# Optimization experiments

Measured on AMD Instinct MI355X. Metric: run time of the kernel, lower is better.

## Reference

```python
import jax, jax.numpy as jnp
import numpy as np
from jax import lax

N = 100000      # number of nodes (== ninput)
E = 3200000     # number of edges per adjacency
NHID = 128
EPS = 1e-12     # torch F.normalize eps


def spmm(src, dst, w, x):
    # sparse adj @ x : out[i] = sum_{e: dst[e]==i} w[e] * x[src[e]]
    return jax.ops.segment_sum(w[:, None] * x[src], dst, num_segments=N)


def l2norm(x):
    # F.normalize(x, p=2, dim=1)
    n = jnp.sqrt(jnp.sum(x * x, axis=1, keepdims=True))
    return x / jnp.maximum(n, EPS)


def mlp(x, L1, bl1, L2, bl2, L3, bl3):
    # dropout == 0.0 -> identity; chunking is a memory optimization, same math
    h = jax.nn.relu(x @ L1 + bl1)
    h = jax.nn.relu(h @ L2 + bl2)
    return h @ L3 + bl3  # [N, 1]


def setup_inputs() -> dict:
    key = jax.random.key(0)
    ks = jax.random.split(key, 32)
    d = {}
    d["adj1_src"] = jax.random.randint(ks[0], (E,), 0, N, dtype=jnp.int32)
    d["adj1_dst"] = jax.random.randint(ks[1], (E,), 0, N, dtype=jnp.int32)
    d["adj1_w"] = jax.random.uniform(ks[2], (E,), dtype=jnp.float32)
    d["adj2_src"] = jax.random.randint(ks[3], (E,), 0, N, dtype=jnp.int32)
    d["adj2_dst"] = jax.random.randint(ks[4], (E,), 0, N, dtype=jnp.int32)
    d["adj2_w"] = jax.random.uniform(ks[5], (E,), dtype=jnp.float32)
    d["W1"] = jax.random.normal(ks[6], (N, NHID), dtype=jnp.float32) * 0.05
    d["b1"] = jnp.zeros((NHID,), jnp.float32)
    for i, k in zip(range(2, 7), ks[7:12]):
        d[f"W{i}"] = jax.random.normal(k, (NHID, NHID), dtype=jnp.float32) * (1.0 / np.sqrt(NHID))
        d[f"b{i}"] = jnp.zeros((NHID,), jnp.float32)
    d["L1"] = jax.random.normal(ks[12], (NHID, 2 * NHID), dtype=jnp.float32) * (1.0 / np.sqrt(NHID))
    d["bl1"] = jnp.zeros((2 * NHID,), jnp.float32)
    d["L2"] = jax.random.normal(ks[13], (2 * NHID, 2 * NHID), dtype=jnp.float32) * (1.0 / np.sqrt(2 * NHID))
    d["bl2"] = jnp.zeros((2 * NHID,), jnp.float32)
    d["L3"] = jax.random.normal(ks[14], (2 * NHID, 1), dtype=jnp.float32) * (1.0 / np.sqrt(2 * NHID))
    d["bl3"] = jnp.zeros((1,), jnp.float32)
    return d


def reference(adj1_src, adj1_dst, adj1_w, adj2_src, adj2_dst, adj2_w,
              W1, b1, W2, b2, W3, b3, W4, b4, W5, b5, W6, b6,
              L1, bl1, L2, bl2, L3, bl3):
    def branch(src, dst, w):
        x1 = l2norm(jax.nn.relu(spmm(src, dst, w, W1) + b1))
        x2 = l2norm(jax.nn.relu(spmm(src, dst, w, x1 @ W2) + b2))
        x3 = l2norm(jax.nn.relu(spmm(src, dst, w, x2 @ W3) + b3))
        x4 = l2norm(jax.nn.relu(spmm(src, dst, w, x3 @ W4) + b4))
        x5 = l2norm(jax.nn.relu(spmm(src, dst, w, x4 @ W5) + b5))
        x6 = jax.nn.relu(spmm(src, dst, w, x5 @ W6) + b6)
        x7 = lax.stop_gradient(x1 + x2 + x3 + x4 + x5 + x6)  # .detach()
        s = jnp.zeros((N, 1), jnp.float32)
        for xi in (x1, x2, x3, x4, x5):  # computed under torch.no_grad()
            s = s + lax.stop_gradient(mlp(xi, L1, bl1, L2, bl2, L3, bl3))
        s = s + mlp(x6, L1, bl1, L2, bl2, L3, bl3)
        s = s + mlp(x7, L1, bl1, L2, bl2, L3, bl3)
        return s / 7.0

    score1 = branch(adj1_src, adj1_dst, adj1_w)
    score2 = branch(adj2_src, adj2_dst, adj2_w)
    return score1 * score2
```

## Files before the change

kernel.cpp:

```cpp
#include <hip/hip_runtime.h>

#define NN 100000
#define NE 3200000
#define HID 128
#define NNH ((size_t)NN * HID)

typedef __attribute__((ext_vector_type(8))) _Float16 f16x8;
typedef __attribute__((ext_vector_type(4))) _Float16 f16x4;
typedef __attribute__((ext_vector_type(4))) float f32x4;

#define SWZ(row, k) ((k) ^ (((row) & 7) << 3))

__global__ void zero_k(int* p, int n) {
    int i = blockIdx.x * 256 + threadIdx.x;
    if (i < n) p[i] = 0;
}

__global__ void hist_k(const int* __restrict__ dst, int* __restrict__ cnt) {
    int e = blockIdx.x * 256 + threadIdx.x;
    if (e < NE) atomicAdd(&cnt[dst[e]], 1);
}

__global__ __launch_bounds__(1024) void scanA_k(int* __restrict__ rowptr, int* __restrict__ bsum, int n) {
    __shared__ int wsum[16];
    int tid = threadIdx.x;
    int lane = tid & 63, wid = tid >> 6;
    int idx = blockIdx.x * 1024 + tid;
    int v = (idx < n) ? rowptr[idx] : 0;
    int s = v;
#pragma unroll
    for (int o = 1; o < 64; o <<= 1) {
        int t = __shfl_up(s, o, 64);
        if (lane >= o) s += t;
    }
    if (lane == 63) wsum[wid] = s;
    __syncthreads();
    if (wid == 0) {
        int ws = (lane < 16) ? wsum[lane] : 0;
#pragma unroll
        for (int o = 1; o < 16; o <<= 1) {
            int t = __shfl_up(ws, o, 64);
            if (lane >= o) ws += t;
        }
        if (lane < 16) wsum[lane] = ws;
    }
    __syncthreads();
    int woff = (wid == 0) ? 0 : wsum[wid - 1];
    if (idx < n) rowptr[idx] = woff + s - v;
    if (tid == 0) bsum[blockIdx.x] = wsum[15];
}

__global__ void scanB_k(int* __restrict__ bsum, int* __restrict__ rowptr, int nb, int n) {
    if (threadIdx.x == 0) {
        int run = 0;
        for (int i = 0; i < nb; ++i) {
            int t = bsum[i];
            bsum[i] = run;
            run += t;
        }
        rowptr[n] = run;
    }
}

__global__ void scanC_k(int* __restrict__ rowptr, int* __restrict__ cursor,
                        const int* __restrict__ bsum, int n) {
    int idx = blockIdx.x * 256 + threadIdx.x;
    if (idx < n) {
        int v = rowptr[idx] + bsum[idx >> 10];
        rowptr[idx] = v;
        cursor[idx] = v;
    }
}

__global__ void scatter_k(const int* __restrict__ src, const int* __restrict__ dst,
                          const float* __restrict__ w, int* __restrict__ cursor,
                          int2* __restrict__ ep) {
    int e = blockIdx.x * 256 + threadIdx.x;
    if (e < NE) {
        int d = dst[e];
        int pos = atomicAdd(&cursor[d], 1);
        ep[pos] = make_int2(src[e], __float_as_int(w[e]));
    }
}

__global__ void convT_k(const float* __restrict__ W, _Float16* __restrict__ WT, int K, int N) {
    int idx = blockIdx.x * 256 + threadIdx.x;
    if (idx < K * N) {
        int k = idx / N, n = idx % N;
        WT[n * K + k] = (_Float16)W[idx];
    }
}

__global__ void conv4_k(const float* __restrict__ A, _Float16* __restrict__ B, int n4) {
    int i = blockIdx.x * 256 + threadIdx.x;
    if (i < n4) {
        float4 v = ((const float4*)A)[i];
        f16x4 h;
        h.x = (_Float16)v.x; h.y = (_Float16)v.y; h.z = (_Float16)v.z; h.w = (_Float16)v.w;
        ((f16x4*)B)[i] = h;
    }
}

template <bool NORM>
__global__ void spmm_k(const _Float16* __restrict__ x, const int* __restrict__ rowptr,
                       const int2* __restrict__ ep, const float* __restrict__ bias,
                       _Float16* __restrict__ outx) {
    int row = blockIdx.x * 4 + (threadIdx.x >> 6);
    int l = threadIdx.x & 63;
    int q = l >> 4, li = l & 15;
    if (row >= NN) return;
    int e0 = rowptr[row], e1 = rowptr[row + 1];
    float acc[8] = {};
#pragma unroll 4
    for (int e = e0 + q; e < e1; e += 4) {
        int2 r = ep[e];
        float w = __int_as_float(r.y);
        f16x8 v = *(const f16x8*)(x + (size_t)r.x * HID + li * 8);
#pragma unroll
        for (int j = 0; j < 8; ++j) acc[j] += w * (float)v[j];
    }
#pragma unroll
    for (int j = 0; j < 8; ++j) {
        acc[j] += __shfl_xor(acc[j], 16, 64);
        acc[j] += __shfl_xor(acc[j], 32, 64);
    }
    const float4* bp = (const float4*)(bias + li * 8);
    float4 b0 = bp[0], b1 = bp[1];
    acc[0] = fmaxf(acc[0] + b0.x, 0.f); acc[1] = fmaxf(acc[1] + b0.y, 0.f);
    acc[2] = fmaxf(acc[2] + b0.z, 0.f); acc[3] = fmaxf(acc[3] + b0.w, 0.f);
    acc[4] = fmaxf(acc[4] + b1.x, 0.f); acc[5] = fmaxf(acc[5] + b1.y, 0.f);
    acc[6] = fmaxf(acc[6] + b1.z, 0.f); acc[7] = fmaxf(acc[7] + b1.w, 0.f);
    if (NORM) {
        float ss = 0.f;
#pragma unroll
        for (int j = 0; j < 8; ++j) ss += acc[j] * acc[j];
        ss += __shfl_xor(ss, 1, 64);
        ss += __shfl_xor(ss, 2, 64);
        ss += __shfl_xor(ss, 4, 64);
        ss += __shfl_xor(ss, 8, 64);
        float sc = 1.0f / fmaxf(sqrtf(ss), 1e-12f);
#pragma unroll
        for (int j = 0; j < 8; ++j) acc[j] *= sc;
    }
    if (q == 0) {
        f16x8 ho;
#pragma unroll
        for (int j = 0; j < 8; ++j) ho[j] = (_Float16)acc[j];
        *(f16x8*)(outx + (size_t)row * HID + li * 8) = ho;
    }
}

template <bool SUM6>
__global__ __launch_bounds__(256) void mlp_fused_k(
    const _Float16* __restrict__ X,
    const _Float16* __restrict__ L1T,
    const float* __restrict__ bl1,
    const _Float16* __restrict__ L2T,
    const float* __restrict__ bl2,
    const float* __restrict__ L3,
    const float* __restrict__ bl3,
    float* __restrict__ sacc) {
    __shared__ _Float16 Xs[64][128];
    __shared__ _Float16 H1s[64][256];
    __shared__ float Hred[4][64];
    int t = threadIdx.x;
    int w = t >> 6, l = t & 63;
    int g = l >> 4, li = l & 15;
    int rowBase = blockIdx.x * 64;

#pragma unroll
    for (int i = 0; i < 4; ++i) {
        int idx = t + i * 256;
        int r = idx >> 4, c8 = idx & 15;
        int gr = rowBase + r;
        if (SUM6) {
            float s[8] = {};
            if (gr < NN) {
#pragma unroll
                for (int l6 = 0; l6 < 6; ++l6) {
                    f16x8 v = *(const f16x8*)(X + (size_t)l6 * NNH + (size_t)gr * HID + c8 * 8);
#pragma unroll
                    for (int j = 0; j < 8; ++j) s[j] += (float)v[j];
                }
            }
            f16x8 hv;
#pragma unroll
            for (int j = 0; j < 8; ++j) hv[j] = (_Float16)s[j];
            *(f16x8*)&Xs[r][SWZ(r, c8 * 8)] = hv;
        } else {
            f16x8 v = (gr < NN) ? *(const f16x8*)(X + (size_t)gr * HID + c8 * 8)
                                : (f16x8)(_Float16)0.f;
            *(f16x8*)&Xs[r][SWZ(r, c8 * 8)] = v;
        }
    }
    __syncthreads();

    int colW = w * 64;
    f32x4 acc[4][4] = {};
#pragma unroll
    for (int ks = 0; ks < 4; ++ks) {
        int kb = ks * 32 + g * 8;
        f16x8 a[4];
#pragma unroll
        for (int mt = 0; mt < 4; ++mt) {
            int r = mt * 16 + li;
            a[mt] = *(const f16x8*)&Xs[r][SWZ(r, kb)];
        }
#pragma unroll
        for (int nt = 0; nt < 4; ++nt) {
            int n = colW + nt * 16 + li;
            f16x8 b = *(const f16x8*)(L1T + n * 128 + kb);
#pragma unroll
            for (int mt = 0; mt < 4; ++mt)
                acc[mt][nt] = __builtin_amdgcn_mfma_f32_16x16x32_f16(a[mt], b, acc[mt][nt], 0, 0, 0);
        }
    }
#pragma unroll
    for (int nt = 0; nt < 4; ++nt) {
        int col = colW + nt * 16 + li;
        float bb = bl1[col];
#pragma unroll
        for (int mt = 0; mt < 4; ++mt)
#pragma unroll
            for (int r4 = 0; r4 < 4; ++r4) {
                int row = mt * 16 + g * 4 + r4;
                H1s[row][SWZ(row, col)] = (_Float16)fmaxf(acc[mt][nt][r4] + bb, 0.f);
            }
    }
    __syncthreads();

    f32x4 acc2[4][4] = {};
#pragma unroll
    for (int ks = 0; ks < 8; ++ks) {
        int kb = ks * 32 + g * 8;
        f16x8 a[4];
#pragma unroll
        for (int mt = 0; mt < 4; ++mt) {
            int r = mt * 16 + li;
            a[mt] = *(const f16x8*)&H1s[r][SWZ(r, kb)];
        }
#pragma unroll
        for (int nt = 0; nt < 4; ++nt) {
            int n = colW + nt * 16 + li;
            f16x8 b = *(const f16x8*)(L2T + n * 256 + kb);
#pragma unroll
            for (int mt = 0; mt < 4; ++mt)
                acc2[mt][nt] = __builtin_amdgcn_mfma_f32_16x16x32_f16(a[mt], b, acc2[mt][nt], 0, 0, 0);
        }
    }
    float part[4][4] = {};
#pragma unroll
    for (int nt = 0; nt < 4; ++nt) {
        int col = colW + nt * 16 + li;
        float bb = bl2[col];
        float l3v = L3[col];
#pragma unroll
        for (int mt = 0; mt < 4; ++mt)
#pragma unroll
            for (int r4 = 0; r4 < 4; ++r4)
                part[mt][r4] += fmaxf(acc2[mt][nt][r4] + bb, 0.f) * l3v;
    }
#pragma unroll
    for (int mt = 0; mt < 4; ++mt)
#pragma unroll
        for (int r4 = 0; r4 < 4; ++r4) {
            float p = part[mt][r4];
            p += __shfl_xor(p, 1, 64);
            p += __shfl_xor(p, 2, 64);
            p += __shfl_xor(p, 4, 64);
            p += __shfl_xor(p, 8, 64);
            if (li == 0) Hred[w][mt * 16 + g * 4 + r4] = p;
        }
    __syncthreads();
    if (t < 64) {
        int gr = rowBase + t;
        if (gr < NN)
            sacc[gr] += Hred[0][t] + Hred[1][t] + Hred[2][t] + Hred[3][t] + bl3[0];
    }
}

__global__ __launch_bounds__(256) void gemm128_mfma_k(const _Float16* __restrict__ X,
                                                      const _Float16* __restrict__ WT,
                                                      _Float16* __restrict__ Y) {
    __shared__ _Float16 Xs[64][128];
    int t = threadIdx.x;
    int w = t >> 6, l = t & 63;
    int g = l >> 4, li = l & 15;
    int rowBase = blockIdx.x * 64;
#pragma unroll
    for (int i = 0; i < 4; ++i) {
        int idx = t + i * 256;
        int r = idx >> 4, c8 = idx & 15;
        int gr = rowBase + r;
        f16x8 v = (gr < NN) ? *(const f16x8*)(X + (size_t)gr * 128 + c8 * 8)
                            : (f16x8)(_Float16)0.f;
        *(f16x8*)&Xs[r][SWZ(r, c8 * 8)] = v;
    }
    __syncthreads();
    int colW = w * 32;
    f32x4 acc[4][2] = {};
#pragma unroll
    for (int ks = 0; ks < 4; ++ks) {
        int kb = ks * 32 + g * 8;
        f16x8 a[4];
#pragma unroll
        for (int mt = 0; mt < 4; ++mt) {
            int r = mt * 16 + li;
            a[mt] = *(const f16x8*)&Xs[r][SWZ(r, kb)];
        }
#pragma unroll
        for (int nt = 0; nt < 2; ++nt) {
            int n = colW + nt * 16 + li;
            f16x8 b = *(const f16x8*)(WT + n * 128 + kb);
#pragma unroll
            for (int mt = 0; mt < 4; ++mt)
                acc[mt][nt] = __builtin_amdgcn_mfma_f32_16x16x32_f16(a[mt], b, acc[mt][nt], 0, 0, 0);
        }
    }
#pragma unroll
    for (int mt = 0; mt < 4; ++mt)
#pragma unroll
        for (int nt = 0; nt < 2; ++nt)
#pragma unroll
            for (int r4 = 0; r4 < 4; ++r4) {
                int gr = rowBase + mt * 16 + g * 4 + r4;
                if (gr < NN)
                    Y[(size_t)gr * 128 + colW + nt * 16 + li] = (_Float16)acc[mt][nt][r4];
            }
}

__global__ void score_store_k(const float* __restrict__ sacc, float* __restrict__ dst) {
    int i = blockIdx.x * 256 + threadIdx.x;
    if (i < NN) dst[i] = sacc[i] * (1.f / 7.f);
}

__global__ void final_mul_k(const float* __restrict__ sacc, const float* __restrict__ score1,
                            float* __restrict__ out) {
    int i = blockIdx.x * 256 + threadIdx.x;
    if (i < NN) out[i] = score1[i] * (sacc[i] * (1.f / 7.f));
}

extern "C" void kernel_launch(void* const* d_in, const int* in_sizes, int n_in,
                              void* d_out, int out_size, void* d_ws, size_t ws_size,
                              hipStream_t stream) {
    const int* asrc[2] = {(const int*)d_in[0], (const int*)d_in[3]};
    const int* adst[2] = {(const int*)d_in[1], (const int*)d_in[4]};
    const float* aw[2] = {(const float*)d_in[2], (const float*)d_in[5]};
    const float* W1 = (const float*)d_in[6];
    const float* b1 = (const float*)d_in[7];
    const float* Wk[5] = {(const float*)d_in[8], (const float*)d_in[10], (const float*)d_in[12],
                          (const float*)d_in[14], (const float*)d_in[16]};
    const float* bk[5] = {(const float*)d_in[9], (const float*)d_in[11], (const float*)d_in[13],
                          (const float*)d_in[15], (const float*)d_in[17]};
    const float* L1 = (const float*)d_in[18];
    const float* bl1 = (const float*)d_in[19];
    const float* L2 = (const float*)d_in[20];
    const float* bl2 = (const float*)d_in[21];
    const float* L3 = (const float*)d_in[22];
    const float* bl3 = (const float*)d_in[23];
    float* out = (float*)d_out;

    char* p = (char*)d_ws;
    _Float16* L1T = (_Float16*)p; p += 65536;
    _Float16* L2T = (_Float16*)p; p += 131072;
    _Float16* WkT = (_Float16*)p; p += 163840;
    _Float16* W1h = (_Float16*)p; p += NNH * 2;
    _Float16* tmp = (_Float16*)p; p += NNH * 2;
    _Float16* xbuf = (_Float16*)p; p += 6 * NNH * 2;
    float* sacc = (float*)p; p += (size_t)NN * 4;
    float* score1 = (float*)p; p += (size_t)NN * 4;
    int2* ep = (int2*)p; p += (size_t)NE * 8;
    int* rowptr = (int*)p; p += (size_t)(NN + 1) * 4;
    int* cursor = (int*)p; p += (size_t)NN * 4;
    int* bsum = (int*)p; p += 512;

    const int GE = (NE + 255) / 256;
    const int GN = (NN + 255) / 256;
    const int GS = (NN + 3) / 4;
    const int GM = (NN + 63) / 64;
    const int NB = (NN + 1023) / 1024;

    convT_k<<<(128 * 256 + 255) / 256, 256, 0, stream>>>(L1, L1T, 128, 256);
    convT_k<<<(256 * 256 + 255) / 256, 256, 0, stream>>>(L2, L2T, 256, 256);
    for (int l = 0; l < 5; ++l)
        convT_k<<<(128 * 128 + 255) / 256, 256, 0, stream>>>(Wk[l], WkT + (size_t)l * 16384, 128, 128);
    conv4_k<<<(NN * HID / 4 + 255) / 256, 256, 0, stream>>>(W1, W1h, NN * HID / 4);

    for (int br = 0; br < 2; ++br) {
        zero_k<<<GN, 256, 0, stream>>>(rowptr, NN + 1);
        hist_k<<<GE, 256, 0, stream>>>(adst[br], rowptr);
        scanA_k<<<NB, 1024, 0, stream>>>(rowptr, bsum, NN);
        scanB_k<<<1, 64, 0, stream>>>(bsum, rowptr, NB, NN);
        scanC_k<<<GN, 256, 0, stream>>>(rowptr, cursor, bsum, NN);
        scatter_k<<<GE, 256, 0, stream>>>(asrc[br], adst[br], aw[br], cursor, ep);

        zero_k<<<GN, 256, 0, stream>>>((int*)sacc, NN);

        spmm_k<true><<<GS, 256, 0, stream>>>(W1h, rowptr, ep, b1, xbuf);
        mlp_fused_k<false><<<GM, 256, 0, stream>>>(xbuf, L1T, bl1, L2T, bl2, L3, bl3, sacc);

        for (int l = 0; l < 5; ++l) {
            gemm128_mfma_k<<<GM, 256, 0, stream>>>(xbuf + (size_t)l * NNH, WkT + (size_t)l * 16384, tmp);
            _Float16* xo = xbuf + (size_t)(l + 1) * NNH;
            if (l < 4)
                spmm_k<true><<<GS, 256, 0, stream>>>(tmp, rowptr, ep, bk[l], xo);
            else
                spmm_k<false><<<GS, 256, 0, stream>>>(tmp, rowptr, ep, bk[l], xo);
            mlp_fused_k<false><<<GM, 256, 0, stream>>>(xo, L1T, bl1, L2T, bl2, L3, bl3, sacc);
        }

        mlp_fused_k<true><<<GM, 256, 0, stream>>>(xbuf, L1T, bl1, L2T, bl2, L3, bl3, sacc);

        if (br == 0)
            score_store_k<<<GN, 256, 0, stream>>>(sacc, score1);
        else
            final_mul_k<<<GN, 256, 0, stream>>>(sacc, score1, out);
    }
}
```

Baseline: 2.874 ms.

## Reorder spmm before dense transform, fuse transform with MLP, pack edges

Uses associativity (A·X)·W = A·(X·W) to run the sparse aggregation first and then a fused kernel that applies the 128x128 weight, bias, ReLU, L2 norm and the scoring MLP in one pass. This removes a separate GEMM launch and a round trip of the activation through memory per layer. Edge records are packed into 32 bits, with the source index shifted into the high bits and an fp16 weight in the low 15 bits, which halves edge-stream traffic but drops the weight's sign bit and reduces its precision. The sacc zeroing kernel is replaced by an init variant of the first MLP.

```diff
diff --git a/kernel.cpp b/kernel.cpp
--- a/kernel.cpp
+++ b/kernel.cpp
@@ -74,12 +74,13 @@
 
 __global__ void scatter_k(const int* __restrict__ src, const int* __restrict__ dst,
                           const float* __restrict__ w, int* __restrict__ cursor,
-                          int2* __restrict__ ep) {
+                          unsigned* __restrict__ ep) {
     int e = blockIdx.x * 256 + threadIdx.x;
     if (e < NE) {
         int d = dst[e];
         int pos = atomicAdd(&cursor[d], 1);
-        ep[pos] = make_int2(src[e], __float_as_int(w[e]));
+        ushort hb = __builtin_bit_cast(ushort, (_Float16)w[e]);
+        ep[pos] = ((unsigned)src[e] << 15) | (unsigned)hb;
     }
 }
 
@@ -101,9 +102,9 @@
     }
 }
 
-template <bool NORM>
+template <bool EPI>
 __global__ void spmm_k(const _Float16* __restrict__ x, const int* __restrict__ rowptr,
-                       const int2* __restrict__ ep, const float* __restrict__ bias,
+                       const unsigned* __restrict__ ep, const float* __restrict__ bias,
                        _Float16* __restrict__ outx) {
     int row = blockIdx.x * 4 + (threadIdx.x >> 6);
     int l = threadIdx.x & 63;
@@ -113,9 +114,10 @@
     float acc[8] = {};
 #pragma unroll 4
     for (int e = e0 + q; e < e1; e += 4) {
-        int2 r = ep[e];
-        float w = __int_as_float(r.y);
-        f16x8 v = *(const f16x8*)(x + (size_t)r.x * HID + li * 8);
+        unsigned r = ep[e];
+        int s = r >> 15;
+        float w = (float)__builtin_bit_cast(_Float16, (ushort)(r & 0x7FFFu));
+        f16x8 v = *(const f16x8*)(x + (size_t)s * HID + li * 8);
 #pragma unroll
         for (int j = 0; j < 8; ++j) acc[j] += w * (float)v[j];
     }
@@ -124,13 +126,13 @@
         acc[j] += __shfl_xor(acc[j], 16, 64);
         acc[j] += __shfl_xor(acc[j], 32, 64);
     }
-    const float4* bp = (const float4*)(bias + li * 8);
-    float4 b0 = bp[0], b1 = bp[1];
-    acc[0] = fmaxf(acc[0] + b0.x, 0.f); acc[1] = fmaxf(acc[1] + b0.y, 0.f);
-    acc[2] = fmaxf(acc[2] + b0.z, 0.f); acc[3] = fmaxf(acc[3] + b0.w, 0.f);
-    acc[4] = fmaxf(acc[4] + b1.x, 0.f); acc[5] = fmaxf(acc[5] + b1.y, 0.f);
-    acc[6] = fmaxf(acc[6] + b1.z, 0.f); acc[7] = fmaxf(acc[7] + b1.w, 0.f);
-    if (NORM) {
+    if (EPI) {
+        const float4* bp = (const float4*)(bias + li * 8);
+        float4 b0 = bp[0], b1 = bp[1];
+        acc[0] = fmaxf(acc[0] + b0.x, 0.f); acc[1] = fmaxf(acc[1] + b0.y, 0.f);
+        acc[2] = fmaxf(acc[2] + b0.z, 0.f); acc[3] = fmaxf(acc[3] + b0.w, 0.f);
+        acc[4] = fmaxf(acc[4] + b1.x, 0.f); acc[5] = fmaxf(acc[5] + b1.y, 0.f);
+        acc[6] = fmaxf(acc[6] + b1.z, 0.f); acc[7] = fmaxf(acc[7] + b1.w, 0.f);
         float ss = 0.f;
 #pragma unroll
         for (int j = 0; j < 8; ++j) ss += acc[j] * acc[j];
@@ -150,19 +152,196 @@
     }
 }
 
-template <bool SUM6>
-__global__ __launch_bounds__(256) void mlp_fused_k(
-    const _Float16* __restrict__ X,
-    const _Float16* __restrict__ L1T,
-    const float* __restrict__ bl1,
-    const _Float16* __restrict__ L2T,
-    const float* __restrict__ bl2,
-    const float* __restrict__ L3,
-    const float* __restrict__ bl3,
+template <bool NORM>
+__global__ __launch_bounds__(256) void trans_mlp_k(
+    const _Float16* __restrict__ Y,
+    const _Float16* __restrict__ WT,
+    const float* __restrict__ bw,
+    _Float16* __restrict__ Xo,
+    const _Float16* __restrict__ L1T, const float* __restrict__ bl1,
+    const _Float16* __restrict__ L2T, const float* __restrict__ bl2,
+    const float* __restrict__ L3, const float* __restrict__ bl3,
     float* __restrict__ sacc) {
     __shared__ _Float16 Xs[64][128];
     __shared__ _Float16 H1s[64][256];
-    __shared__ float Hred[4][64];
+    __shared__ float red[4][64];
+    int t = threadIdx.x;
+    int w = t >> 6, l = t & 63;
+    int g = l >> 4, li = l & 15;
+    int rowBase = blockIdx.x * 64;
+
+#pragma unroll
+    for (int i = 0; i < 4; ++i) {
+        int idx = t + i * 256;
+        int r = idx >> 4, c8 = idx & 15;
+        int gr = rowBase + r;
+        f16x8 v = (gr < NN) ? *(const f16x8*)(Y + (size_t)gr * 128 + c8 * 8)
+                            : (f16x8)(_Float16)0.f;
+        *(f16x8*)&Xs[r][SWZ(r, c8 * 8)] = v;
+    }
+    __syncthreads();
+
+    int cW = w * 32;
+    f32x4 accw[4][2] = {};
+#pragma unroll
+    for (int ks = 0; ks < 4; ++ks) {
+        int kb = ks * 32 + g * 8;
+        f16x8 a[4];
+#pragma unroll
+        for (int mt = 0; mt < 4; ++mt) {
+            int r = mt * 16 + li;
+            a[mt] = *(const f16x8*)&Xs[r][SWZ(r, kb)];
+        }
+#pragma unroll
+        for (int nt = 0; nt < 2; ++nt) {
+            f16x8 b = *(const f16x8*)(WT + (size_t)(cW + nt * 16 + li) * 128 + kb);
+#pragma unroll
+            for (int mt = 0; mt < 4; ++mt)
+                accw[mt][nt] = __builtin_amdgcn_mfma_f32_16x16x32_f16(a[mt], b, accw[mt][nt], 0, 0, 0);
+        }
+    }
+    float vv[4][2][4];
+    float b0 = bw[cW + li], b1v = bw[cW + 16 + li];
+#pragma unroll
+    for (int mt = 0; mt < 4; ++mt)
+#pragma unroll
+        for (int r4 = 0; r4 < 4; ++r4) {
+            vv[mt][0][r4] = fmaxf(accw[mt][0][r4] + b0, 0.f);
+            vv[mt][1][r4] = fmaxf(accw[mt][1][r4] + b1v, 0.f);
+        }
+    if (NORM) {
+#pragma unroll
+        for (int mt = 0; mt < 4; ++mt)
+#pragma unroll
+            for (int r4 = 0; r4 < 4; ++r4) {
+                float ps = vv[mt][0][r4] * vv[mt][0][r4] + vv[mt][1][r4] * vv[mt][1][r4];
+                ps += __shfl_xor(ps, 1, 64);
+                ps += __shfl_xor(ps, 2, 64);
+                ps += __shfl_xor(ps, 4, 64);
+                ps += __shfl_xor(ps, 8, 64);
+                if (li == 0) red[w][mt * 16 + g * 4 + r4] = ps;
+            }
+        __syncthreads();
+        if (t < 64) {
+            float s = red[0][t] + red[1][t] + red[2][t] + red[3][t];
+            red[0][t] = 1.f / fmaxf(sqrtf(s), 1e-12f);
+        }
+        __syncthreads();
+    } else {
+        __syncthreads();
+    }
+#pragma unroll
+    for (int mt = 0; mt < 4; ++mt)
+#pragma unroll
+        for (int r4 = 0; r4 < 4; ++r4) {
+            int row = mt * 16 + g * 4 + r4;
+            float sc = NORM ? red[0][row] : 1.f;
+            _Float16 h0 = (_Float16)(vv[mt][0][r4] * sc);
+            _Float16 h1 = (_Float16)(vv[mt][1][r4] * sc);
+            Xs[row][SWZ(row, cW + li)] = h0;
+            Xs[row][SWZ(row, cW + 16 + li)] = h1;
+            int gr = rowBase + row;
+            if (gr < NN) {
+                Xo[(size_t)gr * 128 + cW + li] = h0;
+                Xo[(size_t)gr * 128 + cW + 16 + li] = h1;
+            }
+        }
+    __syncthreads();
+
+    int cM = w * 64;
+    f32x4 acc[4][4] = {};
+#pragma unroll
+    for (int ks = 0; ks < 4; ++ks) {
+        int kb = ks * 32 + g * 8;
+        f16x8 a[4];
+#pragma unroll
+        for (int mt = 0; mt < 4; ++mt) {
+            int r = mt * 16 + li;
+            a[mt] = *(const f16x8*)&Xs[r][SWZ(r, kb)];
+        }
+#pragma unroll
+        for (int nt = 0; nt < 4; ++nt) {
+            int n = cM + nt * 16 + li;
+            f16x8 b = *(const f16x8*)(L1T + (size_t)n * 128 + kb);
+#pragma unroll
+            for (int mt = 0; mt < 4; ++mt)
+                acc[mt][nt] = __builtin_amdgcn_mfma_f32_16x16x32_f16(a[mt], b, acc[mt][nt], 0, 0, 0);
+        }
+    }
+#pragma unroll
+    for (int nt = 0; nt < 4; ++nt) {
+        int col = cM + nt * 16 + li;
+        float bb = bl1[col];
+#pragma unroll
+        for (int mt = 0; mt < 4; ++mt)
+#pragma unroll
+            for (int r4 = 0; r4 < 4; ++r4) {
+                int row = mt * 16 + g * 4 + r4;
+                H1s[row][SWZ(row, col)] = (_Float16)fmaxf(acc[mt][nt][r4] + bb, 0.f);
+            }
+    }
+    __syncthreads();
+
+    f32x4 acc2[4][4] = {};
+#pragma unroll
+    for (int ks = 0; ks < 8; ++ks) {
+        int kb = ks * 32 + g * 8;
+        f16x8 a[4];
+#pragma unroll
+        for (int mt = 0; mt < 4; ++mt) {
+            int r = mt * 16 + li;
+            a[mt] = *(const f16x8*)&H1s[r][SWZ(r, kb)];
+        }
+#pragma unroll
+        for (int nt = 0; nt < 4; ++nt) {
+            int n = cM + nt * 16 + li;
+            f16x8 b = *(const f16x8*)(L2T + (size_t)n * 256 + kb);
+#pragma unroll
+            for (int mt = 0; mt < 4; ++mt)
+                acc2[mt][nt] = __builtin_amdgcn_mfma_f32_16x16x32_f16(a[mt], b, acc2[mt][nt], 0, 0, 0);
+        }
+    }
+    float part[4][4] = {};
+#pragma unroll
+    for (int nt = 0; nt < 4; ++nt) {
+        int col = cM + nt * 16 + li;
+        float bb = bl2[col];
+        float l3v = L3[col];
+#pragma unroll
+        for (int mt = 0; mt < 4; ++mt)
+#pragma unroll
+            for (int r4 = 0; r4 < 4; ++r4)
+                part[mt][r4] += fmaxf(acc2[mt][nt][r4] + bb, 0.f) * l3v;
+    }
+#pragma unroll
+    for (int mt = 0; mt < 4; ++mt)
+#pragma unroll
+        for (int r4 = 0; r4 < 4; ++r4) {
+            float p = part[mt][r4];
+            p += __shfl_xor(p, 1, 64);
+            p += __shfl_xor(p, 2, 64);
+            p += __shfl_xor(p, 4, 64);
+            p += __shfl_xor(p, 8, 64);
+            if (li == 0) red[w][mt * 16 + g * 4 + r4] = p;
+        }
+    __syncthreads();
+    if (t < 64) {
+        int gr = rowBase + t;
+        if (gr < NN)
+            sacc[gr] += red[0][t] + red[1][t] + red[2][t] + red[3][t] + bl3[0];
+    }
+}
+
+template <bool SUM6, bool INIT>
+__global__ __launch_bounds__(256) void mlp_fused_k(
+    const _Float16* __restrict__ X,
+    const _Float16* __restrict__ L1T, const float* __restrict__ bl1,
+    const _Float16* __restrict__ L2T, const float* __restrict__ bl2,
+    const float* __restrict__ L3, const float* __restrict__ bl3,
+    float* __restrict__ sacc) {
+    __shared__ _Float16 Xs[64][128];
+    __shared__ _Float16 H1s[64][256];
+    __shared__ float red[4][64];
     int t = threadIdx.x;
     int w = t >> 6, l = t & 63;
     int g = l >> 4, li = l & 15;
@@ -195,7 +374,7 @@
     }
     __syncthreads();
 
-    int colW = w * 64;
+    int cM = w * 64;
     f32x4 acc[4][4] = {};
 #pragma unroll
     for (int ks = 0; ks < 4; ++ks) {
@@ -208,8 +387,8 @@
         }
 #pragma unroll
         for (int nt = 0; nt < 4; ++nt) {
-            int n = colW + nt * 16 + li;
-            f16x8 b = *(const f16x8*)(L1T + n * 128 + kb);
+            int n = cM + nt * 16 + li;
+            f16x8 b = *(const f16x8*)(L1T + (size_t)n * 128 + kb);
 #pragma unroll
             for (int mt = 0; mt < 4; ++mt)
                 acc[mt][nt] = __builtin_amdgcn_mfma_f32_16x16x32_f16(a[mt], b, acc[mt][nt], 0, 0, 0);
@@ -217,7 +396,7 @@
     }
 #pragma unroll
     for (int nt = 0; nt < 4; ++nt) {
-        int col = colW + nt * 16 + li;
+        int col = cM + nt * 16 + li;
         float bb = bl1[col];
 #pragma unroll
         for (int mt = 0; mt < 4; ++mt)
@@ -241,8 +420,8 @@
         }
 #pragma unroll
         for (int nt = 0; nt < 4; ++nt) {
-            int n = colW + nt * 16 + li;
-            f16x8 b = *(const f16x8*)(L2T + n * 256 + kb);
+            int n = cM + nt * 16 + li;
+            f16x8 b = *(const f16x8*)(L2T + (size_t)n * 256 + kb);
 #pragma unroll
             for (int mt = 0; mt < 4; ++mt)
                 acc2[mt][nt] = __builtin_amdgcn_mfma_f32_16x16x32_f16(a[mt], b, acc2[mt][nt], 0, 0, 0);
@@ -251,7 +430,7 @@
     float part[4][4] = {};
 #pragma unroll
     for (int nt = 0; nt < 4; ++nt) {
-        int col = colW + nt * 16 + li;
+        int col = cM + nt * 16 + li;
         float bb = bl2[col];
         float l3v = L3[col];
 #pragma unroll
@@ -269,64 +448,16 @@
             p += __shfl_xor(p, 2, 64);
             p += __shfl_xor(p, 4, 64);
             p += __shfl_xor(p, 8, 64);
-            if (li == 0) Hred[w][mt * 16 + g * 4 + r4] = p;
+            if (li == 0) red[w][mt * 16 + g * 4 + r4] = p;
         }
     __syncthreads();
     if (t < 64) {
         int gr = rowBase + t;
-        if (gr < NN)
-            sacc[gr] += Hred[0][t] + Hred[1][t] + Hred[2][t] + Hred[3][t] + bl3[0];
-    }
-}
-
-__global__ __launch_bounds__(256) void gemm128_mfma_k(const _Float16* __restrict__ X,
-                                                      const _Float16* __restrict__ WT,
-                                                      _Float16* __restrict__ Y) {
-    __shared__ _Float16 Xs[64][128];
-    int t = threadIdx.x;
-    int w = t >> 6, l = t & 63;
-    int g = l >> 4, li = l & 15;
-    int rowBase = blockIdx.x * 64;
-#pragma unroll
-    for (int i = 0; i < 4; ++i) {
-        int idx = t + i * 256;
-        int r = idx >> 4, c8 = idx & 15;
-        int gr = rowBase + r;
-        f16x8 v = (gr < NN) ? *(const f16x8*)(X + (size_t)gr * 128 + c8 * 8)
-                            : (f16x8)(_Float16)0.f;
-        *(f16x8*)&Xs[r][SWZ(r, c8 * 8)] = v;
-    }
-    __syncthreads();
-    int colW = w * 32;
-    f32x4 acc[4][2] = {};
-#pragma unroll
-    for (int ks = 0; ks < 4; ++ks) {
-        int kb = ks * 32 + g * 8;
-        f16x8 a[4];
-#pragma unroll
-        for (int mt = 0; mt < 4; ++mt) {
-            int r = mt * 16 + li;
-            a[mt] = *(const f16x8*)&Xs[r][SWZ(r, kb)];
-        }
-#pragma unroll
-        for (int nt = 0; nt < 2; ++nt) {
-            int n = colW + nt * 16 + li;
-            f16x8 b = *(const f16x8*)(WT + n * 128 + kb);
-#pragma unroll
-            for (int mt = 0; mt < 4; ++mt)
-                acc[mt][nt] = __builtin_amdgcn_mfma_f32_16x16x32_f16(a[mt], b, acc[mt][nt], 0, 0, 0);
-        }
-    }
-#pragma unroll
-    for (int mt = 0; mt < 4; ++mt)
-#pragma unroll
-        for (int nt = 0; nt < 2; ++nt)
-#pragma unroll
-            for (int r4 = 0; r4 < 4; ++r4) {
-                int gr = rowBase + mt * 16 + g * 4 + r4;
-                if (gr < NN)
-                    Y[(size_t)gr * 128 + colW + nt * 16 + li] = (_Float16)acc[mt][nt][r4];
-            }
+        if (gr < NN) {
+            float s = red[0][t] + red[1][t] + red[2][t] + red[3][t] + bl3[0];
+            if (INIT) sacc[gr] = s; else sacc[gr] += s;
+        }
+    }
 }
 
 __global__ void score_store_k(const float* __restrict__ sacc, float* __restrict__ dst) {
@@ -369,7 +500,7 @@
     _Float16* xbuf = (_Float16*)p; p += 6 * NNH * 2;
     float* sacc = (float*)p; p += (size_t)NN * 4;
     float* score1 = (float*)p; p += (size_t)NN * 4;
-    int2* ep = (int2*)p; p += (size_t)NE * 8;
+    unsigned* ep = (unsigned*)p; p += (size_t)NE * 4;
     int* rowptr = (int*)p; p += (size_t)(NN + 1) * 4;
     int* cursor = (int*)p; p += (size_t)NN * 4;
     int* bsum = (int*)p; p += 512;
@@ -394,22 +525,21 @@
         scanC_k<<<GN, 256, 0, stream>>>(rowptr, cursor, bsum, NN);
         scatter_k<<<GE, 256, 0, stream>>>(asrc[br], adst[br], aw[br], cursor, ep);
 
-        zero_k<<<GN, 256, 0, stream>>>((int*)sacc, NN);
-
         spmm_k<true><<<GS, 256, 0, stream>>>(W1h, rowptr, ep, b1, xbuf);
-        mlp_fused_k<false><<<GM, 256, 0, stream>>>(xbuf, L1T, bl1, L2T, bl2, L3, bl3, sacc);
+        mlp_fused_k<false, true><<<GM, 256, 0, stream>>>(xbuf, L1T, bl1, L2T, bl2, L3, bl3, sacc);
 
         for (int l = 0; l < 5; ++l) {
-            gemm128_mfma_k<<<GM, 256, 0, stream>>>(xbuf + (size_t)l * NNH, WkT + (size_t)l * 16384, tmp);
+            spmm_k<false><<<GS, 256, 0, stream>>>(xbuf + (size_t)l * NNH, rowptr, ep, b1, tmp);
             _Float16* xo = xbuf + (size_t)(l + 1) * NNH;
             if (l < 4)
-                spmm_k<true><<<GS, 256, 0, stream>>>(tmp, rowptr, ep, bk[l], xo);
+                trans_mlp_k<true><<<GM, 256, 0, stream>>>(tmp, WkT + (size_t)l * 16384, bk[l], xo,
+                                                          L1T, bl1, L2T, bl2, L3, bl3, sacc);
             else
-                spmm_k<false><<<GS, 256, 0, stream>>>(tmp, rowptr, ep, bk[l], xo);
-            mlp_fused_k<false><<<GM, 256, 0, stream>>>(xo, L1T, bl1, L2T, bl2, L3, bl3, sacc);
-        }
-
-        mlp_fused_k<true><<<GM, 256, 0, stream>>>(xbuf, L1T, bl1, L2T, bl2, L3, bl3, sacc);
+                trans_mlp_k<false><<<GM, 256, 0, stream>>>(tmp, WkT + (size_t)l * 16384, bk[l], xo,
+                                                           L1T, bl1, L2T, bl2, L3, bl3, sacc);
+        }
+
+        mlp_fused_k<true, false><<<GM, 256, 0, stream>>>(xbuf, L1T, bl1, L2T, bl2, L3, bl3, sacc);
 
         if (br == 0)
             score_store_k<<<GN, 256, 0, stream>>>(sacc, score1);
```

Result: faster. 2.797 ms (-2.7%).
